# Optimization experiments

Measured on AMD Instinct MI355X. Metric: run time of the kernel, lower is better.

The kernel has to match this reference:

```python
import jax, jax.numpy as jnp
import numpy as np

N = 100000
E = 600000
D = 128


def setup_inputs() -> dict:
    key = jax.random.key(0)
    k_h, k_src, k_dst, k_W, k_b, k_H = jax.random.split(key, 6)
    h = jax.random.normal(k_h, (N, D), dtype=jnp.float32)
    src = jax.random.randint(k_src, (E,), 0, N, dtype=jnp.int64)
    dst = jax.random.randint(k_dst, (E,), 0, N, dtype=jnp.int64)
    # Linear layer params (PyTorch convention: y = x @ W_w.T + W_b)
    bound_lin = 1.0 / np.sqrt(D)
    W_w = jax.random.uniform(k_W, (D, D), dtype=jnp.float32, minval=-bound_lin, maxval=bound_lin)
    W_b = jax.random.uniform(k_b, (D,), dtype=jnp.float32, minval=-bound_lin, maxval=bound_lin)
    # H = normal(0, 1/D) + I
    H = jax.random.normal(k_H, (D, D), dtype=jnp.float32) * (1.0 / D) + jnp.eye(D, dtype=jnp.float32)
    return {"h": h, "src": src, "dst": dst, "W_w": W_w, "W_b": W_b, "H": H}


def reference(h, src, dst, W_w, W_b, H):
    # node transform: hp = W(h)
    hp = h @ W_w.T + W_b  # [N, D]
    # precompute hp @ H at node level (equivalent to (hp[dst]) @ H, cheaper)
    hpH = hp @ H  # [N, D]
    diff = hp[src] - hpH[dst]  # [E, D] edge-wise gather + sub
    score = jnp.sum(diff * diff, axis=-1)  # [E]
    return score
```

## Files before the change

### kernel.cpp

```cpp
#include <hip/hip_runtime.h>
#include <hip/hip_bf16.h>


#define D 128
#define BN 256
#define BM 64

typedef __attribute__((ext_vector_type(8))) short bf16x8;
typedef __attribute__((ext_vector_type(4))) float f32x4;

static __device__ inline unsigned short f2bf(float x) {
  union { float f; unsigned int u; } v;
  v.f = x;
  unsigned int r = v.u + 0x7fffu + ((v.u >> 16) & 1u);
  return (unsigned short)(r >> 16);
}

__global__ __launch_bounds__(128) void prep_kernel(
    const float* __restrict__ Ww, const float* __restrict__ Wb,
    const float* __restrict__ H, float* __restrict__ Wcat,
    float* __restrict__ bias_cat) {
  const int j = blockIdx.x;
  const int a = threadIdx.x;
  if (j < D) {
    Wcat[a * BN + j] = Ww[j * D + a];
    if (a == 0) bias_cat[j] = Wb[j];
  } else {
    const int jj = j - D;
    float acc = 0.f;
#pragma unroll 8
    for (int m = 0; m < D; ++m)
      acc = fmaf(Ww[m * D + a], H[m * D + jj], acc);
    Wcat[a * BN + j] = acc;
    if (a == 0) {
      float cc = 0.f;
#pragma unroll 8
      for (int m = 0; m < D; ++m) cc = fmaf(Wb[m], H[m * D + jj], cc);
      bias_cat[j] = cc;
    }
  }
}

__global__ __launch_bounds__(256) void pack_kernel(
    const float* __restrict__ Wcat, short* __restrict__ Wfrag) {
  const int f = blockIdx.x * 256 + threadIdx.x;
  const int lane = f & 63;
  const int ks = (f >> 6) & 3;
  const int jt = (f >> 8) & 3;
  const int w = f >> 10;
  const int j = w * 64 + jt * 16 + (lane & 15);
  const int kb = ks * 32 + (lane >> 4) * 8;
  unsigned short u[8];
#pragma unroll
  for (int i = 0; i < 8; ++i) u[i] = f2bf(Wcat[(kb + i) * BN + j]);
  *(uint4*)(Wfrag + (size_t)f * 8) = *(const uint4*)u;
}

__global__ __launch_bounds__(256, 4) void phase1_mfma(
    const float* __restrict__ h, const short* __restrict__ Wfrag,
    const float* __restrict__ bias_cat, short* __restrict__ hp,
    short* __restrict__ hpH, int n_nodes) {
  __shared__ short Hf[1024 * 8];

  const int tid = threadIdx.x;
  const int lane = tid & 63;
  const int w = tid >> 6;
  const int base = blockIdx.x * BM;

#pragma unroll
  for (int i = 0; i < 4; ++i) {
    const int f = tid + i * 256;
    const int fl = f & 63;
    const int nt = (f >> 6) & 3;
    const int ks = f >> 8;
    int node = base + nt * 16 + (fl & 15);
    if (node >= n_nodes) node = n_nodes - 1;
    const int kb = ks * 32 + (fl >> 4) * 8;
    const float4 lo = *(const float4*)(h + (size_t)node * D + kb);
    const float4 hi = *(const float4*)(h + (size_t)node * D + kb + 4);
    unsigned short u[8];
    u[0] = f2bf(lo.x); u[1] = f2bf(lo.y); u[2] = f2bf(lo.z); u[3] = f2bf(lo.w);
    u[4] = f2bf(hi.x); u[5] = f2bf(hi.y); u[6] = f2bf(hi.z); u[7] = f2bf(hi.w);
    ((uint4*)Hf)[f] = *(const uint4*)u;
  }

  f32x4 acc[4][4];
#pragma unroll
  for (int jt = 0; jt < 4; ++jt) {
    const float4 b4 =
        *(const float4*)(bias_cat + w * 64 + jt * 16 + ((lane >> 4) << 2));
    const f32x4 bi = {b4.x, b4.y, b4.z, b4.w};
#pragma unroll
    for (int nt = 0; nt < 4; ++nt) acc[jt][nt] = bi;
  }

  __syncthreads();

  const bf16x8* Wf = (const bf16x8*)Wfrag;
  const bf16x8* Hf8 = (const bf16x8*)Hf;
#pragma unroll
  for (int jt = 0; jt < 4; ++jt) {
    bf16x8 wf[4];
#pragma unroll
    for (int ks = 0; ks < 4; ++ks)
      wf[ks] = Wf[(((w * 4 + jt) * 4 + ks) << 6) + lane];
#pragma unroll
    for (int nt = 0; nt < 4; ++nt) {
#pragma unroll
      for (int ks = 0; ks < 4; ++ks) {
        const bf16x8 hf = Hf8[((ks << 2) + nt) * 64 + lane];
        acc[jt][nt] = __builtin_amdgcn_mfma_f32_16x16x32_bf16(
            wf[ks], hf, acc[jt][nt], 0, 0, 0);
      }
    }
  }

  short* outb = (w < 2) ? hp : hpH;
  const int jb = (w & 1) * 64 + ((lane >> 4) << 2);
#pragma unroll
  for (int jt = 0; jt < 4; ++jt) {
#pragma unroll
    for (int nt = 0; nt < 4; ++nt) {
      const int node = base + nt * 16 + (lane & 15);
      if (node < n_nodes) {
        uint2 pk;
        pk.x = (unsigned int)f2bf(acc[jt][nt][0]) |
               ((unsigned int)f2bf(acc[jt][nt][1]) << 16);
        pk.y = (unsigned int)f2bf(acc[jt][nt][2]) |
               ((unsigned int)f2bf(acc[jt][nt][3]) << 16);
        *(uint2*)(outb + (size_t)node * D + jb + jt * 16) = pk;
      }
    }
  }
}

__global__ __launch_bounds__(256) void edge_kernel(
    const short* __restrict__ hp, const short* __restrict__ hpH,
    const int* __restrict__ src, const int* __restrict__ dst,
    float* __restrict__ score, int n_edges) {
  const int lane = threadIdx.x & 15;
  const int e = (blockIdx.x * 256 + threadIdx.x) >> 4;
  if (e >= n_edges) return;

  const int s = src[e];
  const int d = dst[e];
  const uint4 av = *(const uint4*)(hp + (size_t)s * D + lane * 8);
  const uint4 bv = *(const uint4*)(hpH + (size_t)d * D + lane * 8);

  const unsigned int au[4] = {av.x, av.y, av.z, av.w};
  const unsigned int bu[4] = {bv.x, bv.y, bv.z, bv.w};
  float acc = 0.f;
#pragma unroll
  for (int i = 0; i < 4; ++i) {
    const float alo = __uint_as_float(au[i] << 16);
    const float ahi = __uint_as_float(au[i] & 0xffff0000u);
    const float blo = __uint_as_float(bu[i] << 16);
    const float bhi = __uint_as_float(bu[i] & 0xffff0000u);
    float t = alo - blo;
    acc = fmaf(t, t, acc);
    t = ahi - bhi;
    acc = fmaf(t, t, acc);
  }

  acc += __shfl_xor(acc, 1, 64);
  acc += __shfl_xor(acc, 2, 64);
  acc += __shfl_xor(acc, 4, 64);
  acc += __shfl_xor(acc, 8, 64);

  if (lane == 0) __builtin_nontemporal_store(acc, &score[e]);
}

extern "C" void kernel_launch(void* const* d_in, const int* in_sizes, int n_in,
                              void* d_out, int out_size, void* d_ws,
                              size_t ws_size, hipStream_t stream) {
  const float* h = (const float*)d_in[0];
  const int* src = (const int*)d_in[1];
  const int* dst = (const int*)d_in[2];
  const float* Ww = (const float*)d_in[3];
  const float* Wb = (const float*)d_in[4];
  const float* H = (const float*)d_in[5];
  float* score = (float*)d_out;

  const int n_nodes = in_sizes[0] / D;
  const int n_edges = in_sizes[1];

  char* ws = (char*)d_ws;
  short* hp = (short*)ws;
  short* hpH = hp + (size_t)n_nodes * D;
  short* Wfrag = hpH + (size_t)n_nodes * D;
  float* Wcat = (float*)(Wfrag + 4096 * 8);
  float* bias_cat = Wcat + D * BN;

  prep_kernel<<<dim3(BN), dim3(D), 0, stream>>>(Ww, Wb, H, Wcat, bias_cat);
  pack_kernel<<<dim3(16), dim3(256), 0, stream>>>(Wcat, Wfrag);

  const int nblk = (n_nodes + BM - 1) / BM;
  phase1_mfma<<<dim3(nblk), dim3(256), 0, stream>>>(h, Wfrag, bias_cat, hp,
                                                    hpH, n_nodes);

  const int eblk = (n_edges * 16 + 255) / 256;
  edge_kernel<<<dim3(eblk), dim3(256), 0, stream>>>(hp, hpH, src, dst, score,
                                                    n_edges);
}
```

Before: 165.3 us.

## Fuse weight prep and packing; load h directly into MFMA registers without LDS

The prep and pack kernels are merged into one kernel that computes W and W·H directly in MFMA fragment layout, removing a kernel launch and the fp32 Wcat intermediate. The phase1 kernel drops its shared-memory staging and __syncthreads, instead loading and converting h rows straight into per-wave bf16 fragments, with the loop reordered by k-step. Each of the 4 waves now loads the full h tile redundantly from global/L2 (4x more h traffic) in exchange for no LDS and higher potential occupancy. The fused prep kernel runs on only 16 blocks with a serial 128-step loop per thread.

```diff
diff --git a/kernel.cpp b/kernel.cpp
--- a/kernel.cpp
+++ b/kernel.cpp
@@ -16,74 +16,69 @@
   return (unsigned short)(r >> 16);
 }
 
-__global__ __launch_bounds__(128) void prep_kernel(
+__global__ __launch_bounds__(256) void prep_frag_kernel(
     const float* __restrict__ Ww, const float* __restrict__ Wb,
-    const float* __restrict__ H, float* __restrict__ Wcat,
+    const float* __restrict__ H, short* __restrict__ Wfrag,
     float* __restrict__ bias_cat) {
-  const int j = blockIdx.x;
-  const int a = threadIdx.x;
-  if (j < D) {
-    Wcat[a * BN + j] = Ww[j * D + a];
-    if (a == 0) bias_cat[j] = Wb[j];
+  const int b = blockIdx.x;
+  const int w = b >> 2;
+  const int jt = b & 3;
+  const int tid = threadIdx.x;
+  const int ks = tid >> 6;
+  const int lane = tid & 63;
+  const int j = w * 64 + jt * 16 + (lane & 15);
+  const int kb = ks * 32 + ((lane >> 4) << 3);
+
+  unsigned short u[8];
+  if (w < 2) {
+    const float4 lo = *(const float4*)(Ww + j * D + kb);
+    const float4 hi = *(const float4*)(Ww + j * D + kb + 4);
+    u[0] = f2bf(lo.x); u[1] = f2bf(lo.y); u[2] = f2bf(lo.z); u[3] = f2bf(lo.w);
+    u[4] = f2bf(hi.x); u[5] = f2bf(hi.y); u[6] = f2bf(hi.z); u[7] = f2bf(hi.w);
   } else {
     const int jj = j - D;
-    float acc = 0.f;
+    float a0 = 0.f, a1 = 0.f, a2 = 0.f, a3 = 0.f;
+    float a4 = 0.f, a5 = 0.f, a6 = 0.f, a7 = 0.f;
 #pragma unroll 8
-    for (int m = 0; m < D; ++m)
-      acc = fmaf(Ww[m * D + a], H[m * D + jj], acc);
-    Wcat[a * BN + j] = acc;
-    if (a == 0) {
-      float cc = 0.f;
+    for (int m = 0; m < D; ++m) {
+      const float hm = H[m * D + jj];
+      const float4 lo = *(const float4*)(Ww + m * D + kb);
+      const float4 hi = *(const float4*)(Ww + m * D + kb + 4);
+      a0 = fmaf(lo.x, hm, a0); a1 = fmaf(lo.y, hm, a1);
+      a2 = fmaf(lo.z, hm, a2); a3 = fmaf(lo.w, hm, a3);
+      a4 = fmaf(hi.x, hm, a4); a5 = fmaf(hi.y, hm, a5);
+      a6 = fmaf(hi.z, hm, a6); a7 = fmaf(hi.w, hm, a7);
+    }
+    u[0] = f2bf(a0); u[1] = f2bf(a1); u[2] = f2bf(a2); u[3] = f2bf(a3);
+    u[4] = f2bf(a4); u[5] = f2bf(a5); u[6] = f2bf(a6); u[7] = f2bf(a7);
+  }
+  const int F = ((w * 4 + jt) * 4 + ks) * 64 + lane;
+  *(uint4*)(Wfrag + (size_t)F * 8) = *(const uint4*)u;
+
+  if (tid < 16) {
+    const int jb = w * 64 + jt * 16 + tid;
+    float bv;
+    if (w < 2) {
+      bv = Wb[jb];
+    } else {
+      bv = 0.f;
+      const int jj = jb - D;
 #pragma unroll 8
-      for (int m = 0; m < D; ++m) cc = fmaf(Wb[m], H[m * D + jj], cc);
-      bias_cat[j] = cc;
-    }
-  }
-}
-
-__global__ __launch_bounds__(256) void pack_kernel(
-    const float* __restrict__ Wcat, short* __restrict__ Wfrag) {
-  const int f = blockIdx.x * 256 + threadIdx.x;
-  const int lane = f & 63;
-  const int ks = (f >> 6) & 3;
-  const int jt = (f >> 8) & 3;
-  const int w = f >> 10;
-  const int j = w * 64 + jt * 16 + (lane & 15);
-  const int kb = ks * 32 + (lane >> 4) * 8;
-  unsigned short u[8];
-#pragma unroll
-  for (int i = 0; i < 8; ++i) u[i] = f2bf(Wcat[(kb + i) * BN + j]);
-  *(uint4*)(Wfrag + (size_t)f * 8) = *(const uint4*)u;
+      for (int m = 0; m < D; ++m) bv = fmaf(Wb[m], H[m * D + jj], bv);
+    }
+    bias_cat[jb] = bv;
+  }
 }
 
 __global__ __launch_bounds__(256, 4) void phase1_mfma(
     const float* __restrict__ h, const short* __restrict__ Wfrag,
     const float* __restrict__ bias_cat, short* __restrict__ hp,
     short* __restrict__ hpH, int n_nodes) {
-  __shared__ short Hf[1024 * 8];
-
   const int tid = threadIdx.x;
   const int lane = tid & 63;
   const int w = tid >> 6;
   const int base = blockIdx.x * BM;
 
-#pragma unroll
-  for (int i = 0; i < 4; ++i) {
-    const int f = tid + i * 256;
-    const int fl = f & 63;
-    const int nt = (f >> 6) & 3;
-    const int ks = f >> 8;
-    int node = base + nt * 16 + (fl & 15);
-    if (node >= n_nodes) node = n_nodes - 1;
-    const int kb = ks * 32 + (fl >> 4) * 8;
-    const float4 lo = *(const float4*)(h + (size_t)node * D + kb);
-    const float4 hi = *(const float4*)(h + (size_t)node * D + kb + 4);
-    unsigned short u[8];
-    u[0] = f2bf(lo.x); u[1] = f2bf(lo.y); u[2] = f2bf(lo.z); u[3] = f2bf(lo.w);
-    u[4] = f2bf(hi.x); u[5] = f2bf(hi.y); u[6] = f2bf(hi.z); u[7] = f2bf(hi.w);
-    ((uint4*)Hf)[f] = *(const uint4*)u;
-  }
-
   f32x4 acc[4][4];
 #pragma unroll
   for (int jt = 0; jt < 4; ++jt) {
@@ -94,23 +89,33 @@
     for (int nt = 0; nt < 4; ++nt) acc[jt][nt] = bi;
   }
 
-  __syncthreads();
-
   const bf16x8* Wf = (const bf16x8*)Wfrag;
-  const bf16x8* Hf8 = (const bf16x8*)Hf;
-#pragma unroll
-  for (int jt = 0; jt < 4; ++jt) {
-    bf16x8 wf[4];
-#pragma unroll
-    for (int ks = 0; ks < 4; ++ks)
-      wf[ks] = Wf[(((w * 4 + jt) * 4 + ks) << 6) + lane];
+  const int kb = (lane >> 4) << 3;
+
+#pragma unroll
+  for (int ks = 0; ks < 4; ++ks) {
+    bf16x8 hf[4];
 #pragma unroll
     for (int nt = 0; nt < 4; ++nt) {
-#pragma unroll
-      for (int ks = 0; ks < 4; ++ks) {
-        const bf16x8 hf = Hf8[((ks << 2) + nt) * 64 + lane];
+      int node = base + nt * 16 + (lane & 15);
+      if (node >= n_nodes) node = n_nodes - 1;
+      const float* hrow = h + (size_t)node * D + ks * 32 + kb;
+      const float4 lo = *(const float4*)hrow;
+      const float4 hi = *(const float4*)(hrow + 4);
+      union { bf16x8 v; unsigned short u[8]; } pk;
+      pk.u[0] = f2bf(lo.x); pk.u[1] = f2bf(lo.y);
+      pk.u[2] = f2bf(lo.z); pk.u[3] = f2bf(lo.w);
+      pk.u[4] = f2bf(hi.x); pk.u[5] = f2bf(hi.y);
+      pk.u[6] = f2bf(hi.z); pk.u[7] = f2bf(hi.w);
+      hf[nt] = pk.v;
+    }
+#pragma unroll
+    for (int jt = 0; jt < 4; ++jt) {
+      const bf16x8 wf = Wf[(((w * 4 + jt) * 4 + ks) << 6) + lane];
+#pragma unroll
+      for (int nt = 0; nt < 4; ++nt) {
         acc[jt][nt] = __builtin_amdgcn_mfma_f32_16x16x32_bf16(
-            wf[ks], hf, acc[jt][nt], 0, 0, 0);
+            wf, hf[nt], acc[jt][nt], 0, 0, 0);
       }
     }
   }
@@ -188,11 +193,10 @@
   short* hp = (short*)ws;
   short* hpH = hp + (size_t)n_nodes * D;
   short* Wfrag = hpH + (size_t)n_nodes * D;
-  float* Wcat = (float*)(Wfrag + 4096 * 8);
-  float* bias_cat = Wcat + D * BN;
-
-  prep_kernel<<<dim3(BN), dim3(D), 0, stream>>>(Ww, Wb, H, Wcat, bias_cat);
-  pack_kernel<<<dim3(16), dim3(256), 0, stream>>>(Wcat, Wfrag);
+  float* bias_cat = (float*)(Wfrag + 4096 * 8);
+
+  prep_frag_kernel<<<dim3(16), dim3(256), 0, stream>>>(Ww, Wb, H, Wfrag,
+                                                       bias_cat);
 
   const int nblk = (n_nodes + BM - 1) / BM;
   phase1_mfma<<<dim3(nblk), dim3(256), 0, stream>>>(h, Wfrag, bias_cat, hp,
```

After: 188.2 us. 1.14x slower.
